# Optimization experiments

Measured on AMD Instinct MI355X. Metric: run time of the kernel, lower is better.

Reference implementation:

```python
import jax, jax.numpy as jnp
import numpy as np

EMBED_DIM = 1024


def setup_inputs() -> dict:
    key = jax.random.key(0)
    ks = jax.random.split(key, 9)
    d = EMBED_DIM
    s = 1.0 / np.sqrt(d)
    return {
        "x": jax.random.normal(ks[0], (4, 2048, d), dtype=jnp.float32),
        "wq": jax.random.normal(ks[1], (d, d), dtype=jnp.float32) * s,
        "bq": jnp.zeros((d,), dtype=jnp.float32),
        "wk": jax.random.normal(ks[2], (d, d), dtype=jnp.float32) * s,
        "bk": jnp.zeros((d,), dtype=jnp.float32),
        "wv": jax.random.normal(ks[3], (d, d), dtype=jnp.float32) * s,
        "bv": jnp.zeros((d,), dtype=jnp.float32),
        "wo": jax.random.normal(ks[4], (d, d), dtype=jnp.float32) * s,
        "bo": jnp.zeros((d,), dtype=jnp.float32),
    }


def reference(x, wq, bq, wk, bk, wv, bv, wo, bo):
    # x: [B, S, D]; weights stored as [D_in, D_out] (torch Linear applies x @ W.T,
    # here we fold the transpose into storage).
    d = x.shape[-1]
    q = x @ wq + bq
    k = x @ wk + bk
    v = x @ wv + bv
    scores = jnp.einsum('bqd,bkd->bqk', q, k) / jnp.sqrt(jnp.float32(d))
    attn = jax.nn.softmax(scores, axis=-1)
    out = jnp.einsum('bqk,bkd->bqd', attn, v)
    return out @ wo + bo
```

## Files before the change

kernel.cpp:

```cpp
#include <hip/hip_runtime.h>
#include <stdint.h>

typedef __attribute__((ext_vector_type(4))) float f32x4;
typedef __attribute__((ext_vector_type(8))) short short8v;
typedef __attribute__((ext_vector_type(4))) unsigned short ushort4v;
typedef __attribute__((ext_vector_type(8))) unsigned short ushort8v;

__device__ __forceinline__ unsigned short f2b(float x) {
  union { float f; unsigned int u; } c; c.f = x;
  unsigned int r = (c.u + 0x7fffu + ((c.u >> 16) & 1u)) >> 16;
  return (unsigned short)r;
}

__device__ __forceinline__ void gload_lds16(const void* g, void* l) {
  __builtin_amdgcn_global_load_lds(
      (const __attribute__((address_space(1))) void*)g,
      (__attribute__((address_space(3))) void*)l, 16, 0, 0);
}

__device__ __forceinline__ f32x4 MFMA16(short8v a, short8v b, f32x4 c) {
  return __builtin_amdgcn_mfma_f32_16x16x32_bf16(a, b, c, 0, 0, 0);
}

template <int N>
__device__ __forceinline__ void wvm() {
  if constexpr (N == 8) asm volatile("s_waitcnt vmcnt(8)" ::: "memory");
  else if constexpr (N == 6) asm volatile("s_waitcnt vmcnt(6)" ::: "memory");
  else if constexpr (N == 4) asm volatile("s_waitcnt vmcnt(4)" ::: "memory");
  else if constexpr (N == 3) asm volatile("s_waitcnt vmcnt(3)" ::: "memory");
  else asm volatile("s_waitcnt vmcnt(0)" ::: "memory");
}

__global__ __launch_bounds__(256) void cvt_bf16(const float* __restrict__ in,
                                                unsigned short* __restrict__ out,
                                                int n8) {
  for (int i = blockIdx.x * 256 + threadIdx.x; i < n8; i += gridDim.x * 256) {
    f32x4 a = *((const f32x4*)in + (size_t)i * 2);
    f32x4 b = *((const f32x4*)in + (size_t)i * 2 + 1);
    ushort8v o;
    o[0] = f2b(a[0]); o[1] = f2b(a[1]); o[2] = f2b(a[2]); o[3] = f2b(a[3]);
    o[4] = f2b(b[0]); o[5] = f2b(b[1]); o[6] = f2b(b[2]); o[7] = f2b(b[3]);
    *((ushort8v*)out + i) = o;
  }
}

__global__ __launch_bounds__(256) void wt4_bf16(const float* __restrict__ w0,
                                                const float* __restrict__ w1,
                                                const float* __restrict__ w2,
                                                const float* __restrict__ w3,
                                                unsigned short* __restrict__ o0,
                                                unsigned short* __restrict__ o1,
                                                unsigned short* __restrict__ o2,
                                                unsigned short* __restrict__ o3) {
  const int z = blockIdx.z;
  const float* W = z == 0 ? w0 : z == 1 ? w1 : z == 2 ? w2 : w3;
  unsigned short* WT = z == 0 ? o0 : z == 1 ? o1 : z == 2 ? o2 : o3;
  __shared__ float t[64][65];
  const int bi = blockIdx.y * 64, bj = blockIdx.x * 64;
#pragma unroll
  for (int i = 0; i < 16; ++i) {
    int idx = i * 256 + threadIdx.x;
    int r = idx >> 6, c = idx & 63;
    t[r][c] = W[(size_t)(bi + r) * 1024 + bj + c];
  }
  __syncthreads();
#pragma unroll
  for (int i = 0; i < 16; ++i) {
    int idx = i * 256 + threadIdx.x;
    int r = idx >> 6, c = idx & 63;
    WT[(size_t)(bj + r) * 1024 + bi + c] = f2b(t[c][r]);
  }
}

__global__ __launch_bounds__(256) void softmax_rows(float* __restrict__ S,
                                                    long long bstride) {
  float* row = S + (long long)blockIdx.y * bstride + (size_t)blockIdx.x * 2048;
  const int t = threadIdx.x;
  f32x4 a = *(const f32x4*)(row + t * 8);
  f32x4 b = *(const f32x4*)(row + t * 8 + 4);
  float m = fmaxf(fmaxf(fmaxf(a[0], a[1]), fmaxf(a[2], a[3])),
                  fmaxf(fmaxf(b[0], b[1]), fmaxf(b[2], b[3])));
#pragma unroll
  for (int o = 32; o; o >>= 1) m = fmaxf(m, __shfl_xor(m, o));
  __shared__ float red[4];
  const int wid = t >> 6, lane = t & 63;
  if (lane == 0) red[wid] = m;
  __syncthreads();
  m = fmaxf(fmaxf(red[0], red[1]), fmaxf(red[2], red[3]));
  float e[8];
  float s = 0.f;
#pragma unroll
  for (int j = 0; j < 4; ++j) { e[j] = __expf(a[j] - m); s += e[j]; }
#pragma unroll
  for (int j = 0; j < 4; ++j) { e[4 + j] = __expf(b[j] - m); s += e[4 + j]; }
#pragma unroll
  for (int o = 32; o; o >>= 1) s += __shfl_xor(s, o);
  __syncthreads();
  if (lane == 0) red[wid] = s;
  __syncthreads();
  s = red[0] + red[1] + red[2] + red[3];
  const float inv = 1.f / s;
  ushort8v o8;
#pragma unroll
  for (int j = 0; j < 8; ++j) o8[j] = f2b(e[j] * inv);
  __syncthreads();
  *((ushort8v*)row + t) = o8;
}

template <int EPI, int BM>
__global__ __launch_bounds__(512, 2) void gemm256(
    const unsigned short* __restrict__ A, int lda,
    const unsigned short* __restrict__ B, int ldb,
    void* __restrict__ C0, void* __restrict__ C1, void* __restrict__ C2,
    int ldc, const float* __restrict__ bias0, const float* __restrict__ bias1,
    const float* __restrict__ bias2, float scale, int K,
    long long bsA, long long bsB, long long bsC) {
  extern __shared__ __align__(16) char smem[];
  constexpr int ABY = BM * 64;
  constexpr int KHS = ABY + 16384;
  constexpr int SBUF = 2 * KHS;
  constexpr int MF = BM / 32;
  constexpr int FH = MF / 2;
  constexpr int AL = BM / 128;
  constexpr int L = AL + 2;

  const int tid = threadIdx.x;
  const int z = blockIdx.z;
  A += (long long)z * bsA;
  B += (long long)z * bsB;
  const int blkrow = blockIdx.y * BM, blkcol = blockIdx.x * 256;
  const int lane = tid & 63, wid = tid >> 6;
  const int kblk = lane >> 4, l15 = lane & 15;
  const int arw = (wid >> 2) * (BM / 2) + l15;
  const int brw = (wid & 3) * 64 + l15;
  const int aoff = arw * 64 + ((kblk ^ ((arw >> 1) & 3)) << 4);
  const int boff = ABY + brw * 64 + ((kblk ^ ((brw >> 1) & 3)) << 4);
  const int srow = tid >> 2;
  const int scc = (((tid & 3) ^ ((srow >> 1) & 3)) << 3);
  const unsigned short* ag = A + (size_t)(blkrow + srow) * lda + scc;
  const unsigned short* bg = B + (size_t)(blkcol + srow) * ldb + scc;

  auto stA = [&](char* buf, int kt, int kh) {
    const unsigned short* g = ag + kt * 64 + kh * 32;
    char* l = buf + kh * KHS + tid * 16;
#pragma unroll
    for (int rr = 0; rr < AL; ++rr)
      gload_lds16(g + (size_t)(rr * 128) * lda, l + rr * 8192);
  };
  auto stB = [&](char* buf, int kt, int kh) {
    const unsigned short* g = bg + kt * 64 + kh * 32;
    char* l = buf + ABY + kh * KHS + tid * 16;
    gload_lds16(g, l);
    gload_lds16(g + (size_t)128 * ldb, l + 8192);
  };

  f32x4 acc[MF][4] = {};
  short8v af[4], bf[4];

#define LDAH(BUF, KK, MB)                                                     \
  { _Pragma("unroll") for (int m_ = 0; m_ < FH; ++m_)                         \
      af[m_] = *(const short8v*)((BUF) + (KK)*KHS + aoff + ((MB) + m_) * 1024); }
#define LDB4(BUF, KK)                                                         \
  { _Pragma("unroll") for (int n_ = 0; n_ < 4; ++n_)                          \
      bf[n_] = *(const short8v*)((BUF) + (KK)*KHS + boff + n_ * 1024); }
#define MMH(MH)                                                               \
  { _Pragma("unroll") for (int m_ = 0; m_ < FH; ++m_)                         \
      _Pragma("unroll") for (int n_ = 0; n_ < 4; ++n_)                        \
        acc[(MH)*FH + m_][n_] = MFMA16(af[m_], bf[n_], acc[(MH)*FH + m_][n_]); }
#define BAR __builtin_amdgcn_s_barrier()
#define WLGKM0 asm volatile("s_waitcnt lgkmcnt(0)" ::: "memory")

  const int NT = K >> 6;
  stA(smem, 0, 0); stB(smem, 0, 0); stA(smem, 0, 1); stB(smem, 0, 1);
  wvm<L>();
  BAR;
  for (int t = 0; t < NT; ++t) {
    char* cur = smem + (t & 1) * SBUF;
    char* nxt = smem + ((t + 1) & 1) * SBUF;
    const bool pf = (t + 1 < NT);
    LDAH(cur, 0, 0);
    LDB4(cur, 0);
    if (pf) { stA(nxt, t + 1, 0); stB(nxt, t + 1, 0); }
    BAR; WLGKM0;
    __builtin_amdgcn_s_setprio(1);
    MMH(0);
    __builtin_amdgcn_s_setprio(0);
    BAR;
    LDAH(cur, 0, FH);
    if (pf) { stA(nxt, t + 1, 1); stB(nxt, t + 1, 1); }
    BAR; WLGKM0;
    __builtin_amdgcn_s_setprio(1);
    MMH(1);
    __builtin_amdgcn_s_setprio(0);
    if (pf) wvm<2 * L>(); else wvm<0>();
    BAR;
    LDAH(cur, 1, 0);
    LDB4(cur, 1);
    BAR; WLGKM0;
    __builtin_amdgcn_s_setprio(1);
    MMH(0);
    __builtin_amdgcn_s_setprio(0);
    BAR;
    LDAH(cur, 1, FH);
    BAR; WLGKM0;
    __builtin_amdgcn_s_setprio(1);
    MMH(1);
    __builtin_amdgcn_s_setprio(0);
    if (pf) wvm<L>();
    BAR;
  }

  const int gr0 = blkrow + (wid >> 2) * (BM / 2) + kblk * 4;
  const int gc0 = blkcol + (wid & 3) * 64 + l15;
  if (EPI == 0) {
    float* C = (float*)C0 + (long long)z * bsC;
#pragma unroll
    for (int mi = 0; mi < MF; ++mi)
#pragma unroll
      for (int n = 0; n < 4; ++n) {
        const int gc = gc0 + n * 16;
        const float badd = bias0 ? bias0[gc] : 0.f;
#pragma unroll
        for (int j = 0; j < 4; ++j)
          C[(size_t)(gr0 + mi * 16 + j) * ldc + gc] = acc[mi][n][j] * scale + badd;
      }
  } else if (EPI == 1) {
    unsigned short* C = (unsigned short*)C0 + (long long)z * bsC;
#pragma unroll
    for (int mi = 0; mi < MF; ++mi)
#pragma unroll
      for (int n = 0; n < 4; ++n) {
        const int gc = gc0 + n * 16;
        const float badd = bias0 ? bias0[gc] : 0.f;
#pragma unroll
        for (int j = 0; j < 4; ++j)
          C[(size_t)(gr0 + mi * 16 + j) * ldc + gc] = f2b(acc[mi][n][j] * scale + badd);
      }
  } else {
    const int seg = blkcol >> 10;
#pragma unroll
    for (int mi = 0; mi < MF; ++mi)
#pragma unroll
      for (int n = 0; n < 4; ++n) {
        const int gc = gc0 + n * 16;
        const int lc = gc - seg * 1024;
        if (seg < 2) {
          unsigned short* O = (unsigned short*)(seg == 0 ? C0 : C1);
          const float* bb = (seg == 0 ? bias0 : bias1);
          const float badd = bb[lc];
#pragma unroll
          for (int j = 0; j < 4; ++j)
            O[(size_t)(gr0 + mi * 16 + j) * 1024 + lc] = f2b(acc[mi][n][j] + badd);
        } else {
          unsigned short* O = (unsigned short*)C2;
          const float badd = bias2[lc];
          ushort4v pk;
#pragma unroll
          for (int j = 0; j < 4; ++j) pk[j] = f2b(acc[mi][n][j] + badd);
          *(ushort4v*)(O + (size_t)lc * 8192 + gr0 + mi * 16) = pk;
        }
      }
  }
#undef LDAH
#undef LDB4
#undef MMH
#undef BAR
#undef WLGKM0
}

template <int OMODE, bool BIAS, bool SCALE>
__global__ __launch_bounds__(256, 2) void gemm_bt(
    const unsigned short* __restrict__ A, int lda,
    const unsigned short* __restrict__ B, int ldb,
    void* __restrict__ Cp, int ldc,
    const float* __restrict__ bias, float scale, int K,
    long long bsA, long long bsB, long long bsC) {
  __shared__ unsigned short As[128 * 32];
  __shared__ unsigned short Bs[128 * 32];
  const int tid = threadIdx.x;
  A += (long long)blockIdx.z * bsA;
  B += (long long)blockIdx.z * bsB;
  const int brow = blockIdx.y * 128, bcol = blockIdx.x * 128;
  const int wid = tid >> 6, lane = tid & 63;
  const int wr = (wid >> 1) * 64, wc = (wid & 1) * 64;
  const int lrow = lane & 15, kblk = lane >> 4;
  f32x4 acc[4][4] = {};
  for (int kk = 0; kk < K; kk += 32) {
#pragma unroll
    for (int r = 0; r < 2; ++r) {
      int idx = r * 256 + tid;
      int row = idx >> 2, seg = (idx & 3) * 8;
      gload_lds16(A + (size_t)(brow + row) * lda + kk + seg, (char*)As + idx * 16);
      gload_lds16(B + (size_t)(bcol + row) * ldb + kk + seg, (char*)Bs + idx * 16);
    }
    __syncthreads();
    short8v af[4], bv[4];
#pragma unroll
    for (int m = 0; m < 4; ++m)
      af[m] = *(const short8v*)(As + (wr + m * 16 + lrow) * 32 + kblk * 8);
#pragma unroll
    for (int n = 0; n < 4; ++n)
      bv[n] = *(const short8v*)(Bs + (wc + n * 16 + lrow) * 32 + kblk * 8);
#pragma unroll
    for (int m = 0; m < 4; ++m)
#pragma unroll
      for (int n = 0; n < 4; ++n)
        acc[m][n] = MFMA16(af[m], bv[n], acc[m][n]);
    __syncthreads();
  }
  const int r0 = brow + wr + kblk * 4;
  const int c0 = bcol + wc + lrow;
  if (OMODE == 0) {
    float* C = (float*)Cp + (long long)blockIdx.z * bsC;
#pragma unroll
    for (int m = 0; m < 4; ++m)
#pragma unroll
      for (int n = 0; n < 4; ++n) {
        const int cc = c0 + n * 16;
        const float badd = BIAS ? bias[cc] : 0.f;
#pragma unroll
        for (int j = 0; j < 4; ++j) {
          float v = acc[m][n][j];
          if (SCALE) v *= scale;
          C[(size_t)(r0 + m * 16 + j) * ldc + cc] = v + badd;
        }
      }
  } else if (OMODE == 1) {
    unsigned short* C = (unsigned short*)Cp + (long long)blockIdx.z * bsC;
#pragma unroll
    for (int m = 0; m < 4; ++m)
#pragma unroll
      for (int n = 0; n < 4; ++n) {
        const int cc = c0 + n * 16;
        const float badd = BIAS ? bias[cc] : 0.f;
#pragma unroll
        for (int j = 0; j < 4; ++j) {
          float v = acc[m][n][j];
          if (SCALE) v *= scale;
          C[(size_t)(r0 + m * 16 + j) * ldc + cc] = f2b(v + badd);
        }
      }
  } else {
    unsigned short* C = (unsigned short*)Cp + (long long)blockIdx.z * bsC;
#pragma unroll
    for (int m = 0; m < 4; ++m)
#pragma unroll
      for (int n = 0; n < 4; ++n) {
        const int cc = c0 + n * 16;
        const float badd = BIAS ? bias[cc] : 0.f;
        ushort4v pk;
#pragma unroll
        for (int j = 0; j < 4; ++j) {
          float v = acc[m][n][j];
          if (SCALE) v *= scale;
          pk[j] = f2b(v + badd);
        }
        *(ushort4v*)(C + (size_t)cc * ldc + (r0 + m * 16)) = pk;
      }
  }
}

extern "C" void kernel_launch(void* const* d_in, const int* in_sizes, int n_in,
                              void* d_out, int out_size, void* d_ws, size_t ws_size,
                              hipStream_t stream) {
  const float* x  = (const float*)d_in[0];
  const float* wq = (const float*)d_in[1];
  const float* bq = (const float*)d_in[2];
  const float* wk = (const float*)d_in[3];
  const float* bk = (const float*)d_in[4];
  const float* wv = (const float*)d_in[5];
  const float* bv = (const float*)d_in[6];
  const float* wo = (const float*)d_in[7];
  const float* bo = (const float*)d_in[8];
  float* out = (float*)d_out;
  char* ws = (char*)d_ws;

  const long long WELEM = 1024LL * 1024;
  const long long BATCH = 2048LL * 1024;
  const long long FULL  = 4 * BATCH;
  const long long SELEM = 2048LL * 2048;

  const size_t need_A = 8388608ull + 5ull * 16777216 + 4ull * 16777216;
  const size_t need_C = 8388608ull + 4ull * 4194304 + 16777216ull;

  if (ws_size >= need_A) {
    unsigned short* wqT = (unsigned short*)ws;
    unsigned short* wkT = wqT + WELEM;
    unsigned short* wvT = wkT + WELEM;
    unsigned short* woT = wvT + WELEM;
    unsigned short* xb  = woT + WELEM;
    unsigned short* qb  = xb + FULL;
    unsigned short* kb  = qb + FULL;
    unsigned short* vt  = kb + FULL;
    unsigned short* ao  = vt + FULL;
    float* S = (float*)(ao + FULL);

    hipFuncSetAttribute(reinterpret_cast<const void*>(&gemm256<2, 256>),
                        hipFuncAttributeMaxDynamicSharedMemorySize, 131072);
    hipFuncSetAttribute(reinterpret_cast<const void*>(&gemm256<0, 256>),
                        hipFuncAttributeMaxDynamicSharedMemorySize, 131072);
    hipFuncSetAttribute(reinterpret_cast<const void*>(&gemm256<1, 128>),
                        hipFuncAttributeMaxDynamicSharedMemorySize, 98304);
    hipFuncSetAttribute(reinterpret_cast<const void*>(&gemm256<0, 128>),
                        hipFuncAttributeMaxDynamicSharedMemorySize, 98304);

    cvt_bf16<<<2048, 256, 0, stream>>>(x, xb, (int)(FULL / 8));
    wt4_bf16<<<dim3(16, 16, 4), 256, 0, stream>>>(wq, wk, wv, wo, wqT, wkT, wvT, woT);

    gemm256<2, 256><<<dim3(12, 32, 1), 512, 131072, stream>>>(
        xb, 1024, wqT, 1024, qb, kb, vt, 0, bq, bk, bv, 1.f, 1024, 0, 0, 0);
    gemm256<0, 256><<<dim3(8, 8, 4), 512, 131072, stream>>>(
        qb, 1024, kb, 1024, S, nullptr, nullptr, 2048, nullptr, nullptr,
        nullptr, 0.03125f, 1024, BATCH, BATCH, SELEM);
    softmax_rows<<<dim3(2048, 4), 256, 0, stream>>>(S, SELEM);
    gemm256<1, 128><<<dim3(4, 16, 4), 512, 98304, stream>>>(
        (const unsigned short*)S, 4096, vt, 8192, ao, nullptr, nullptr, 1024,
        nullptr, nullptr, nullptr, 1.f, 2048, 2 * SELEM, 2048, BATCH);
    gemm256<0, 128><<<dim3(4, 64, 1), 512, 98304, stream>>>(
        ao, 1024, woT, 1024, out, nullptr, nullptr, 1024, bo, nullptr, nullptr,
        1.f, 1024, 0, 0, 0);
  } else if (ws_size >= need_C) {
    unsigned short* wqT = (unsigned short*)ws;
    unsigned short* wkT = wqT + WELEM;
    unsigned short* wvT = wkT + WELEM;
    unsigned short* woT = wvT + WELEM;
    unsigned short* xb  = woT + WELEM;
    unsigned short* qb  = xb + BATCH;
    unsigned short* kb  = qb + BATCH;
    unsigned short* vtb = kb + BATCH;
    float* S = (float*)(vtb + BATCH);

    wt4_bf16<<<dim3(16, 16, 4), 256, 0, stream>>>(wq, wk, wv, wo, wqT, wkT, wvT, woT);

    for (int b = 0; b < 4; ++b) {
      cvt_bf16<<<1024, 256, 0, stream>>>(x + b * BATCH, xb, (int)(BATCH / 8));
      dim3 gqkv(8, 16);
      gemm_bt<1, true, false><<<gqkv, 256, 0, stream>>>(xb, 1024, wqT, 1024, qb, 1024, bq, 1.f, 1024, 0, 0, 0);
      gemm_bt<1, true, false><<<gqkv, 256, 0, stream>>>(xb, 1024, wkT, 1024, kb, 1024, bk, 1.f, 1024, 0, 0, 0);
      gemm_bt<2, true, false><<<gqkv, 256, 0, stream>>>(xb, 1024, wvT, 1024, vtb, 2048, bv, 1.f, 1024, 0, 0, 0);
      gemm_bt<0, false, true><<<dim3(16, 16), 256, 0, stream>>>(
          qb, 1024, kb, 1024, S, 2048, nullptr, 0.03125f, 1024, 0, 0, 0);
      softmax_rows<<<dim3(2048, 1), 256, 0, stream>>>(S, 0);
      gemm_bt<1, false, false><<<dim3(8, 16), 256, 0, stream>>>(
          (const unsigned short*)S, 4096, vtb, 2048, xb, 1024, nullptr, 1.f, 2048, 0, 0, 0);
      gemm_bt<0, true, false><<<dim3(8, 16), 256, 0, stream>>>(
          xb, 1024, woT, 1024, out + b * BATCH, 1024, bo, 1.f, 1024, 0, 0, 0);
    }
  }
}
```

Measured before the change: 229.5 us.

## Store attention scores as bf16, fuse prep kernels, split V projection GEMM

Merges the x conversion and the weight transposes into one prep launch. The QK^T GEMM now writes bf16 scores, and a new bf16 softmax reads and writes them in place, which halves score traffic and lets the PV GEMM read the buffer directly. The fused QKV GEMM is split into a Q/K GEMM plus a separate V GEMM with a transposed-store epilogue. Rounding the scores to bf16 before softmax costs some accuracy, and the fallback path carries an odd local struct and a forward-declared kernel.

```diff
diff --git a/kernel.cpp b/kernel.cpp
--- a/kernel.cpp
+++ b/kernel.cpp
@@ -10,6 +10,11 @@
   union { float f; unsigned int u; } c; c.f = x;
   unsigned int r = (c.u + 0x7fffu + ((c.u >> 16) & 1u)) >> 16;
   return (unsigned short)r;
+}
+
+__device__ __forceinline__ float b2f(unsigned short x) {
+  union { unsigned int u; float f; } c; c.u = ((unsigned int)x) << 16;
+  return c.f;
 }
 
 __device__ __forceinline__ void gload_lds16(const void* g, void* l) {
@@ -31,28 +36,25 @@
   else asm volatile("s_waitcnt vmcnt(0)" ::: "memory");
 }
 
-__global__ __launch_bounds__(256) void cvt_bf16(const float* __restrict__ in,
-                                                unsigned short* __restrict__ out,
-                                                int n8) {
-  for (int i = blockIdx.x * 256 + threadIdx.x; i < n8; i += gridDim.x * 256) {
-    f32x4 a = *((const f32x4*)in + (size_t)i * 2);
-    f32x4 b = *((const f32x4*)in + (size_t)i * 2 + 1);
-    ushort8v o;
-    o[0] = f2b(a[0]); o[1] = f2b(a[1]); o[2] = f2b(a[2]); o[3] = f2b(a[3]);
-    o[4] = f2b(b[0]); o[5] = f2b(b[1]); o[6] = f2b(b[2]); o[7] = f2b(b[3]);
-    *((ushort8v*)out + i) = o;
-  }
-}
-
-__global__ __launch_bounds__(256) void wt4_bf16(const float* __restrict__ w0,
-                                                const float* __restrict__ w1,
-                                                const float* __restrict__ w2,
-                                                const float* __restrict__ w3,
-                                                unsigned short* __restrict__ o0,
-                                                unsigned short* __restrict__ o1,
-                                                unsigned short* __restrict__ o2,
-                                                unsigned short* __restrict__ o3) {
+__global__ __launch_bounds__(256) void prep(
+    const float* __restrict__ x, const float* __restrict__ w0,
+    const float* __restrict__ w1, const float* __restrict__ w2,
+    const float* __restrict__ w3, unsigned short* __restrict__ xb,
+    unsigned short* __restrict__ o0, unsigned short* __restrict__ o1,
+    unsigned short* __restrict__ o2, unsigned short* __restrict__ o3) {
   const int z = blockIdx.z;
+  if (z == 4) {
+    const int linear = blockIdx.y * 16 + blockIdx.x;
+    for (int i = linear * 256 + threadIdx.x; i < 1048576; i += 65536) {
+      f32x4 a = *((const f32x4*)x + (size_t)i * 2);
+      f32x4 b = *((const f32x4*)x + (size_t)i * 2 + 1);
+      ushort8v o;
+      o[0] = f2b(a[0]); o[1] = f2b(a[1]); o[2] = f2b(a[2]); o[3] = f2b(a[3]);
+      o[4] = f2b(b[0]); o[5] = f2b(b[1]); o[6] = f2b(b[2]); o[7] = f2b(b[3]);
+      *((ushort8v*)xb + i) = o;
+    }
+    return;
+  }
   const float* W = z == 0 ? w0 : z == 1 ? w1 : z == 2 ? w2 : w3;
   unsigned short* WT = z == 0 ? o0 : z == 1 ? o1 : z == 2 ? o2 : o3;
   __shared__ float t[64][65];
@@ -70,6 +72,40 @@
     int r = idx >> 6, c = idx & 63;
     WT[(size_t)(bj + r) * 1024 + bi + c] = f2b(t[c][r]);
   }
+}
+
+__global__ __launch_bounds__(256) void softmax_bf16(unsigned short* __restrict__ S,
+                                                    long long bstride) {
+  unsigned short* row = S + (long long)blockIdx.y * bstride + (size_t)blockIdx.x * 2048;
+  const int t = threadIdx.x;
+  ushort8v u = *((const ushort8v*)row + t);
+  float v[8];
+#pragma unroll
+  for (int j = 0; j < 8; ++j) v[j] = b2f(u[j]);
+  float m = v[0];
+#pragma unroll
+  for (int j = 1; j < 8; ++j) m = fmaxf(m, v[j]);
+#pragma unroll
+  for (int o = 32; o; o >>= 1) m = fmaxf(m, __shfl_xor(m, o));
+  __shared__ float red[4];
+  const int wid = t >> 6, lane = t & 63;
+  if (lane == 0) red[wid] = m;
+  __syncthreads();
+  m = fmaxf(fmaxf(red[0], red[1]), fmaxf(red[2], red[3]));
+  float s = 0.f;
+#pragma unroll
+  for (int j = 0; j < 8; ++j) { v[j] = __expf(v[j] - m); s += v[j]; }
+#pragma unroll
+  for (int o = 32; o; o >>= 1) s += __shfl_xor(s, o);
+  __syncthreads();
+  if (lane == 0) red[wid] = s;
+  __syncthreads();
+  s = red[0] + red[1] + red[2] + red[3];
+  const float inv = 1.f / s;
+  ushort8v o8;
+#pragma unroll
+  for (int j = 0; j < 8; ++j) o8[j] = f2b(v[j] * inv);
+  *((ushort8v*)row + t) = o8;
 }
 
 __global__ __launch_bounds__(256) void softmax_rows(float* __restrict__ S,
@@ -236,29 +272,32 @@
         for (int j = 0; j < 4; ++j)
           C[(size_t)(gr0 + mi * 16 + j) * ldc + gc] = f2b(acc[mi][n][j] * scale + badd);
       }
+  } else if (EPI == 2) {
+    const int seg = blkcol >> 10;
+    unsigned short* O = (unsigned short*)(seg == 0 ? C0 : C1);
+    const float* bb = (seg == 0 ? bias0 : bias1);
+#pragma unroll
+    for (int mi = 0; mi < MF; ++mi)
+#pragma unroll
+      for (int n = 0; n < 4; ++n) {
+        const int lc = gc0 + n * 16 - seg * 1024;
+        const float badd = bb[lc];
+#pragma unroll
+        for (int j = 0; j < 4; ++j)
+          O[(size_t)(gr0 + mi * 16 + j) * 1024 + lc] = f2b(acc[mi][n][j] + badd);
+      }
   } else {
-    const int seg = blkcol >> 10;
+    unsigned short* O = (unsigned short*)C2;
 #pragma unroll
     for (int mi = 0; mi < MF; ++mi)
 #pragma unroll
       for (int n = 0; n < 4; ++n) {
         const int gc = gc0 + n * 16;
-        const int lc = gc - seg * 1024;
-        if (seg < 2) {
-          unsigned short* O = (unsigned short*)(seg == 0 ? C0 : C1);
-          const float* bb = (seg == 0 ? bias0 : bias1);
-          const float badd = bb[lc];
-#pragma unroll
-          for (int j = 0; j < 4; ++j)
-            O[(size_t)(gr0 + mi * 16 + j) * 1024 + lc] = f2b(acc[mi][n][j] + badd);
-        } else {
-          unsigned short* O = (unsigned short*)C2;
-          const float badd = bias2[lc];
-          ushort4v pk;
-#pragma unroll
-          for (int j = 0; j < 4; ++j) pk[j] = f2b(acc[mi][n][j] + badd);
-          *(ushort4v*)(O + (size_t)lc * 8192 + gr0 + mi * 16) = pk;
-        }
+        const float badd = bias2[gc];
+        ushort4v pk;
+#pragma unroll
+        for (int j = 0; j < 4; ++j) pk[j] = f2b(acc[mi][n][j] + badd);
+        *(ushort4v*)(O + (size_t)gc * 8192 + gr0 + mi * 16) = pk;
       }
   }
 #undef LDAH
@@ -393,29 +432,35 @@
     unsigned short* kb  = qb + FULL;
     unsigned short* vt  = kb + FULL;
     unsigned short* ao  = vt + FULL;
-    float* S = (float*)(ao + FULL);
+    unsigned short* S   = ao + FULL;
 
     hipFuncSetAttribute(reinterpret_cast<const void*>(&gemm256<2, 256>),
                         hipFuncAttributeMaxDynamicSharedMemorySize, 131072);
-    hipFuncSetAttribute(reinterpret_cast<const void*>(&gemm256<0, 256>),
+    hipFuncSetAttribute(reinterpret_cast<const void*>(&gemm256<3, 128>),
+                        hipFuncAttributeMaxDynamicSharedMemorySize, 98304);
+    hipFuncSetAttribute(reinterpret_cast<const void*>(&gemm256<1, 256>),
                         hipFuncAttributeMaxDynamicSharedMemorySize, 131072);
     hipFuncSetAttribute(reinterpret_cast<const void*>(&gemm256<1, 128>),
                         hipFuncAttributeMaxDynamicSharedMemorySize, 98304);
     hipFuncSetAttribute(reinterpret_cast<const void*>(&gemm256<0, 128>),
                         hipFuncAttributeMaxDynamicSharedMemorySize, 98304);
 
-    cvt_bf16<<<2048, 256, 0, stream>>>(x, xb, (int)(FULL / 8));
-    wt4_bf16<<<dim3(16, 16, 4), 256, 0, stream>>>(wq, wk, wv, wo, wqT, wkT, wvT, woT);
-
-    gemm256<2, 256><<<dim3(12, 32, 1), 512, 131072, stream>>>(
-        xb, 1024, wqT, 1024, qb, kb, vt, 0, bq, bk, bv, 1.f, 1024, 0, 0, 0);
-    gemm256<0, 256><<<dim3(8, 8, 4), 512, 131072, stream>>>(
+    prep<<<dim3(16, 16, 5), 256, 0, stream>>>(x, wq, wk, wv, wo, xb,
+                                              wqT, wkT, wvT, woT);
+
+    gemm256<2, 256><<<dim3(8, 32, 1), 512, 131072, stream>>>(
+        xb, 1024, wqT, 1024, qb, kb, nullptr, 0, bq, bk, nullptr,
+        1.f, 1024, 0, 0, 0);
+    gemm256<3, 128><<<dim3(4, 64, 1), 512, 98304, stream>>>(
+        xb, 1024, wvT, 1024, nullptr, nullptr, vt, 0, nullptr, nullptr, bv,
+        1.f, 1024, 0, 0, 0);
+    gemm256<1, 256><<<dim3(8, 8, 4), 512, 131072, stream>>>(
         qb, 1024, kb, 1024, S, nullptr, nullptr, 2048, nullptr, nullptr,
         nullptr, 0.03125f, 1024, BATCH, BATCH, SELEM);
-    softmax_rows<<<dim3(2048, 4), 256, 0, stream>>>(S, SELEM);
+    softmax_bf16<<<dim3(2048, 4), 256, 0, stream>>>(S, SELEM);
     gemm256<1, 128><<<dim3(4, 16, 4), 512, 98304, stream>>>(
-        (const unsigned short*)S, 4096, vt, 8192, ao, nullptr, nullptr, 1024,
-        nullptr, nullptr, nullptr, 1.f, 2048, 2 * SELEM, 2048, BATCH);
+        S, 2048, vt, 8192, ao, nullptr, nullptr, 1024,
+        nullptr, nullptr, nullptr, 1.f, 2048, SELEM, 2048, BATCH);
     gemm256<0, 128><<<dim3(4, 64, 1), 512, 98304, stream>>>(
         ao, 1024, woT, 1024, out, nullptr, nullptr, 1024, bo, nullptr, nullptr,
         1.f, 1024, 0, 0, 0);
@@ -430,10 +475,15 @@
     unsigned short* vtb = kb + BATCH;
     float* S = (float*)(vtb + BATCH);
 
-    wt4_bf16<<<dim3(16, 16, 4), 256, 0, stream>>>(wq, wk, wv, wo, wqT, wkT, wvT, woT);
+    prep<<<dim3(16, 16, 4), 256, 0, stream>>>(x, wq, wk, wv, wo, xb,
+                                              wqT, wkT, wvT, woT);
 
     for (int b = 0; b < 4; ++b) {
-      cvt_bf16<<<1024, 256, 0, stream>>>(x + b * BATCH, xb, (int)(BATCH / 8));
+      {
+        struct L { static __global__ void k(const float* in, unsigned short* o, int n8); };
+      }
+      extern __global__ void cvt_batch(const float*, unsigned short*, int);
+      cvt_batch<<<1024, 256, 0, stream>>>(x + b * BATCH, xb, (int)(BATCH / 8));
       dim3 gqkv(8, 16);
       gemm_bt<1, true, false><<<gqkv, 256, 0, stream>>>(xb, 1024, wqT, 1024, qb, 1024, bq, 1.f, 1024, 0, 0, 0);
       gemm_bt<1, true, false><<<gqkv, 256, 0, stream>>>(xb, 1024, wkT, 1024, kb, 1024, bk, 1.f, 1024, 0, 0, 0);
@@ -448,3 +498,16 @@
     }
   }
 }
+
+__global__ __launch_bounds__(256) void cvt_batch(const float* __restrict__ in,
+                                                 unsigned short* __restrict__ out,
+                                                 int n8) {
+  for (int i = blockIdx.x * 256 + threadIdx.x; i < n8; i += gridDim.x * 256) {
+    f32x4 a = *((const f32x4*)in + (size_t)i * 2);
+    f32x4 b = *((const f32x4*)in + (size_t)i * 2 + 1);
+    ushort8v o;
+    o[0] = f2b(a[0]); o[1] = f2b(a[1]); o[2] = f2b(a[2]); o[3] = f2b(a[3]);
+    o[4] = f2b(b[0]); o[5] = f2b(b[1]); o[6] = f2b(b[2]); o[7] = f2b(b[3]);
+    *((ushort8v*)out + i) = o;
+  }
+}
```

Result: faster. 208.3 us (-9.2%).
